# Optimization experiments

Hardware: AMD Instinct MI355X
Metric: run time of the kernel (lower is better)

The kernel has to match this reference:

```python
import jax, jax.numpy as jnp
import numpy as np

B, T, C = 4, 2048, 1024
H = 16
D = C // H  # head_dim = 64


def setup_inputs() -> dict:
    key = jax.random.key(0)
    k1, k2, k3, k4, k5 = jax.random.split(key, 5)
    s = 1.0 / np.sqrt(C)
    return {
        "hidden_state": jax.random.normal(k1, (B, T, C), dtype=jnp.float32),
        "qkv_w": jax.random.uniform(k2, (C, 3 * C), jnp.float32, -s, s),
        "qkv_b": jax.random.uniform(k3, (3 * C,), jnp.float32, -s, s),
        "o_w": jax.random.uniform(k4, (C, C), jnp.float32, -s, s),
        "o_b": jax.random.uniform(k5, (C,), jnp.float32, -s, s),
    }


def reference(hidden_state, qkv_w, qkv_b, o_w, o_b):
    Bq, Tq, Cq = hidden_state.shape
    qkv = hidden_state @ qkv_w + qkv_b  # [B,T,3C]
    q, k, v = jnp.split(qkv, 3, axis=-1)
    # [B,T,C] -> [B,H,T,D]
    q = q.reshape(Bq, Tq, H, D).transpose(0, 2, 1, 3)
    k = k.reshape(Bq, Tq, H, D).transpose(0, 2, 1, 3)
    v = v.reshape(Bq, Tq, H, D).transpose(0, 2, 1, 3)
    scaling = D ** (-0.5)
    scores = jnp.einsum("bhqd,bhkd->bhqk", q, k) * scaling  # [B,H,T,T]
    causal = jnp.tril(jnp.ones((Tq, Tq), dtype=bool))
    scores = jnp.where(causal[None, None], scores, -jnp.inf)
    attn = jax.nn.softmax(scores, axis=-1)
    out = jnp.einsum("bhqk,bhkd->bhqd", attn, v)  # [B,H,T,D]
    out = out.transpose(0, 2, 1, 3).reshape(Bq, Tq, Cq)
    return out @ o_w + o_b
```

## Files before the change

kernel.cpp:

```cpp
#include <hip/hip_runtime.h>
#include <hip/hip_bf16.h>

#define Bn 4
#define Tn 2048
#define Cn 1024
#define Hn 16
#define Dn 64
#define Kdim 1024

typedef __bf16 bf16x8 __attribute__((ext_vector_type(8)));
typedef float f32x4 __attribute__((ext_vector_type(4)));
union B8 { uint4 u; bf16x8 f; ushort s[8]; };

static __device__ __forceinline__ ushort f2bf(float x) {
    __hip_bfloat16 h = __float2bfloat16(x);
    return *(ushort*)&h;
}

#define AS1 __attribute__((address_space(1)))
#define AS3 __attribute__((address_space(3)))

static __device__ __forceinline__ void gload_lds16(const ushort* g, ushort* l) {
    __builtin_amdgcn_global_load_lds((AS1 const uint4*)(const void*)g,
                                     (AS3 uint4*)(void*)l, 16, 0, 0);
}

__global__ __launch_bounds__(256) void cvt_bf16(
    const float* __restrict__ src, ushort* __restrict__ dst, int n)
{
    int i = (blockIdx.x * 256 + threadIdx.x) * 8;
    if (i >= n) return;
    float4 a = *(const float4*)&src[i];
    float4 b = *(const float4*)&src[i + 4];
    ushort4 o0, o1;
    o0.x = f2bf(a.x); o0.y = f2bf(a.y); o0.z = f2bf(a.z); o0.w = f2bf(a.w);
    o1.x = f2bf(b.x); o1.y = f2bf(b.y); o1.z = f2bf(b.z); o1.w = f2bf(b.w);
    *(ushort4*)&dst[i] = o0;
    *(ushort4*)&dst[i + 4] = o1;
}

__global__ __launch_bounds__(256) void transpose_bf16(
    const float* __restrict__ W, ushort* __restrict__ Wt, int N)
{
    __shared__ float Ls[32][33];
    const int k0 = blockIdx.y * 32, n0 = blockIdx.x * 32;
    const int tx = threadIdx.x & 31, ty = threadIdx.x >> 5;
    #pragma unroll
    for (int i = 0; i < 4; i++) {
        int r = ty + i * 8;
        Ls[r][tx] = W[(size_t)(k0 + r) * N + n0 + tx];
    }
    __syncthreads();
    #pragma unroll
    for (int i = 0; i < 4; i++) {
        int r = ty + i * 8;
        Wt[(size_t)(n0 + r) * Kdim + k0 + tx] = f2bf(Ls[tx][r]);
    }
}

template <int EPI>
__global__ __launch_bounds__(256) void gemm_bt(
    const ushort* __restrict__ A, const ushort* __restrict__ Bt,
    const float* __restrict__ bias,
    float* __restrict__ Out, ushort* __restrict__ Qb,
    ushort* __restrict__ Kb, ushort* __restrict__ Vtb)
{
    const int m0 = blockIdx.y * 128;
    const int n0 = blockIdx.x * 128;
    const int t  = threadIdx.x;
    const int wave = t >> 6, lane = t & 63;
    const int ln = lane & 15, quad = lane >> 4;
    const int wm = wave >> 1, wn = wave & 1;

    __shared__ ushort As[128 * 64];
    __shared__ ushort Bs[128 * 64];

    f32x4 acc[4][4] = {};

    for (int k0 = 0; k0 < Kdim; k0 += 64) {
        __syncthreads();
        #pragma unroll
        for (int it = 0; it < 4; it++) {
            int c = it * 256 + wave * 64 + lane;
            int row = c >> 3, seg = c & 7;
            int gseg = seg ^ (row & 7);
            gload_lds16(&A [(size_t)(m0 + row) * Kdim + k0 + gseg * 8], &As[c * 8]);
            gload_lds16(&Bt[(size_t)(n0 + row) * Kdim + k0 + gseg * 8], &Bs[c * 8]);
        }
        __syncthreads();

        #pragma unroll
        for (int ks = 0; ks < 2; ks++) {
            bf16x8 af[4], bf[4];
            #pragma unroll
            for (int mm = 0; mm < 4; mm++) {
                int row = wm * 64 + mm * 16 + ln;
                int seg = (ks * 4 + quad) ^ (ln & 7);
                B8 tmp; tmp.u = *(const uint4*)&As[row * 64 + seg * 8];
                af[mm] = tmp.f;
            }
            #pragma unroll
            for (int nn = 0; nn < 4; nn++) {
                int row = wn * 64 + nn * 16 + ln;
                int seg = (ks * 4 + quad) ^ (ln & 7);
                B8 tmp; tmp.u = *(const uint4*)&Bs[row * 64 + seg * 8];
                bf[nn] = tmp.f;
            }
            #pragma unroll
            for (int mm = 0; mm < 4; mm++)
                #pragma unroll
                for (int nn = 0; nn < 4; nn++)
                    acc[mm][nn] = __builtin_amdgcn_mfma_f32_16x16x32_bf16(
                        af[mm], bf[nn], acc[mm][nn], 0, 0, 0);
        }
    }

    if (EPI == 0) {
        #pragma unroll
        for (int nn = 0; nn < 4; nn++) {
            int n = n0 + wn * 64 + nn * 16 + ln;
            float bv = bias[n];
            #pragma unroll
            for (int mm = 0; mm < 4; mm++) {
                int mbase = m0 + wm * 64 + mm * 16 + quad * 4;
                #pragma unroll
                for (int reg = 0; reg < 4; reg++)
                    Out[(size_t)(mbase + reg) * 1024 + n] = acc[mm][nn][reg] + bv;
            }
        }
    } else {
        const int nb = n0 + wn * 64;
        const int which = nb >> 10;
        const int h = (nb & 1023) >> 6;
        const float scale = (which == 0) ? 0.125f * 1.44269504088896f : 1.0f;
        const int b_ = m0 >> 11;
        const int t0 = (m0 & 2047) + wm * 64;

        __syncthreads();
        ushort* tile = ((wave & 2) ? Bs : As) + (wave & 1) * 4096;

        if (which == 2) {
            #pragma unroll
            for (int nn = 0; nn < 4; nn++) {
                float bv = bias[nb + nn * 16 + ln];
                #pragma unroll
                for (int mm = 0; mm < 4; mm++)
                    #pragma unroll
                    for (int reg = 0; reg < 4; reg++) {
                        int m = mm * 16 + quad * 4 + reg;
                        int n = nn * 16 + ln;
                        tile[n * 64 + (m ^ (((n >> 1) & 7) * 8))] =
                            f2bf(acc[mm][nn][reg] + bv);
                    }
            }
            #pragma unroll
            for (int it = 0; it < 8; it++) {
                int idx = it * 64 + lane;
                int row = idx >> 3, seg = idx & 7;
                uint4 v = *(const uint4*)&tile[row * 64 +
                              ((seg * 8) ^ (((row >> 1) & 7) * 8))];
                *(uint4*)&Vtb[((size_t)((b_ * Hn + h) * Dn) + row) * Tn + t0 + seg * 8] = v;
            }
        } else {
            ushort* dst = (which == 0) ? Qb : Kb;
            #pragma unroll
            for (int nn = 0; nn < 4; nn++) {
                float bv = bias[nb + nn * 16 + ln];
                #pragma unroll
                for (int mm = 0; mm < 4; mm++)
                    #pragma unroll
                    for (int reg = 0; reg < 4; reg++) {
                        int m = mm * 16 + quad * 4 + reg;
                        int n = nn * 16 + ln;
                        tile[m * 64 + (n ^ (((m >> 1) & 7) * 8))] =
                            f2bf((acc[mm][nn][reg] + bv) * scale);
                    }
            }
            #pragma unroll
            for (int it = 0; it < 8; it++) {
                int idx = it * 64 + lane;
                int row = idx >> 3, seg = idx & 7;
                uint4 v = *(const uint4*)&tile[row * 64 +
                              ((seg * 8) ^ (((row >> 1) & 7) * 8))];
                *(uint4*)&dst[((size_t)((b_ * Hn + h) * Tn) + t0 + row) * Dn + seg * 8] = v;
            }
        }
    }
}

__global__ __launch_bounds__(256, 2) void attn_mfma(
    const ushort* __restrict__ Qb, const ushort* __restrict__ Kb,
    const ushort* __restrict__ Vtb, ushort* __restrict__ Ob)
{
    const int bh   = blockIdx.x;
    const int qt   = 15 - blockIdx.y;
    const int t    = threadIdx.x;
    const int wave = t >> 6, lane = t & 63;
    const int ln   = lane & 15, quad = lane >> 4;

    __shared__ ushort Ks[2][128 * 64];
    __shared__ ushort Ps[4][32 * 34];

    const ushort* KgB = Kb  + (size_t)bh * Tn * Dn;
    const ushort* VgB = Vtb + (size_t)bh * Dn * Tn;
    const int b_ = bh >> 4, h = bh & 15;

    #define STAGE_K(kc, buf)                                                   \
        do {                                                                   \
            _Pragma("unroll")                                                  \
            for (int it = 0; it < 4; it++) {                                   \
                int c = it * 256 + wave * 64 + lane;                           \
                int row = c >> 3, seg = c & 7;                                 \
                int gs = seg ^ (row & 7);                                      \
                gload_lds16(&KgB[(size_t)((kc) * 128 + row) * Dn + gs * 8],    \
                            &Ks[buf][c * 8]);                                  \
            }                                                                  \
        } while (0)

    int cur = 0;
    STAGE_K(0, 0);

    const int q0 = qt * 128;

    const ushort* Qg = Qb + ((size_t)bh * Tn + q0 + wave * 32) * Dn;
    bf16x8 qf[2][2];
    #pragma unroll
    for (int ns = 0; ns < 2; ns++)
        #pragma unroll
        for (int ks = 0; ks < 2; ks++) {
            B8 tmp; tmp.u = *(const uint4*)&Qg[(ns * 16 + ln) * 64 + ks * 32 + quad * 8];
            qf[ns][ks] = tmp.f;
        }

    f32x4 Oacc[4][2] = {};
    float m_r[2] = {-1e30f, -1e30f}, l_r[2] = {0.f, 0.f};

    for (int kc = 0; kc <= qt; kc++) {
        __syncthreads();

        B8 vfr[4][4];
        #pragma unroll
        for (int gks = 0; gks < 4; gks++)
            #pragma unroll
            for (int ctd = 0; ctd < 4; ctd++)
                vfr[ctd][gks].u = *(const uint4*)&VgB[
                    (size_t)(ctd * 16 + ln) * Tn + kc * 128 + gks * 32 + quad * 8];

        if (kc < qt) STAGE_K(kc + 1, cur ^ 1);

        const ushort* Kc = Ks[cur];
        f32x4 S[8][2] = {};
        #pragma unroll
        for (int ks = 0; ks < 2; ks++)
            #pragma unroll
            for (int ct = 0; ct < 8; ct++) {
                B8 a; a.u = *(const uint4*)&Kc[(ct * 16 + ln) * 64 +
                                               (((ks * 4 + quad) ^ (ln & 7)) * 8)];
                #pragma unroll
                for (int ns = 0; ns < 2; ns++)
                    S[ct][ns] = __builtin_amdgcn_mfma_f32_16x16x32_bf16(
                        a.f, qf[ns][ks], S[ct][ns], 0, 0, 0);
            }

        if (kc == qt) {
            #pragma unroll
            for (int ct = 0; ct < 8; ct++) {
                int keyl = ct * 16 + quad * 4;
                #pragma unroll
                for (int ns = 0; ns < 2; ns++) {
                    int ql = wave * 32 + ns * 16 + ln;
                    #pragma unroll
                    for (int reg = 0; reg < 4; reg++)
                        if (keyl + reg > ql) S[ct][ns][reg] = -1e30f;
                }
            }
        }

        float alpha[2], ssum[2] = {0.f, 0.f};
        #pragma unroll
        for (int ns = 0; ns < 2; ns++) {
            float pm = -1e30f;
            #pragma unroll
            for (int ct = 0; ct < 8; ct++)
                #pragma unroll
                for (int reg = 0; reg < 4; reg++)
                    pm = fmaxf(pm, S[ct][ns][reg]);
            pm = fmaxf(pm, __shfl_xor(pm, 16));
            pm = fmaxf(pm, __shfl_xor(pm, 32));
            float mn = fmaxf(m_r[ns], pm);
            alpha[ns] = exp2f(m_r[ns] - mn);
            m_r[ns] = mn;
            #pragma unroll
            for (int ctd = 0; ctd < 4; ctd++)
                Oacc[ctd][ns] *= alpha[ns];
        }

        ushort* Pw = Ps[wave];
        #pragma unroll
        for (int p = 0; p < 4; p++) {
            #pragma unroll
            for (int ct_h = 0; ct_h < 2; ct_h++) {
                int ct = p * 2 + ct_h;
                #pragma unroll
                for (int ns = 0; ns < 2; ns++) {
                    ushort4 o;
                    #pragma unroll
                    for (int reg = 0; reg < 4; reg++) {
                        float pv = exp2f(S[ct][ns][reg] - m_r[ns]);
                        ssum[ns] += pv;
                        ((ushort*)&o)[reg] = f2bf(pv);
                    }
                    *(ushort4*)&Pw[(ns * 16 + ln) * 34 + ct_h * 16 + quad * 4] = o;
                }
            }
            #pragma unroll
            for (int ns = 0; ns < 2; ns++) {
                B8 pfr; pfr.u = *(const uint4*)&Pw[(ns * 16 + ln) * 34 + quad * 8];
                #pragma unroll
                for (int ctd = 0; ctd < 4; ctd++)
                    Oacc[ctd][ns] = __builtin_amdgcn_mfma_f32_16x16x32_bf16(
                        vfr[ctd][p].f, pfr.f, Oacc[ctd][ns], 0, 0, 0);
            }
        }
        #pragma unroll
        for (int ns = 0; ns < 2; ns++) {
            float s = ssum[ns];
            s += __shfl_xor(s, 16);
            s += __shfl_xor(s, 32);
            l_r[ns] = l_r[ns] * alpha[ns] + s;
        }
        cur ^= 1;
    }

    #pragma unroll
    for (int ns = 0; ns < 2; ns++) {
        float inv = 1.0f / l_r[ns];
        int token = q0 + wave * 32 + ns * 16 + ln;
        ushort* dst = Ob + ((size_t)(b_ * Tn + token)) * Cn + h * 64;
        #pragma unroll
        for (int ctd = 0; ctd < 4; ctd++) {
            ushort4 o;
            #pragma unroll
            for (int reg = 0; reg < 4; reg++)
                ((ushort*)&o)[reg] = f2bf(Oacc[ctd][ns][reg] * inv);
            *(ushort4*)&dst[ctd * 16 + quad * 4] = o;
        }
    }
    #undef STAGE_K
}

extern "C" void kernel_launch(void* const* d_in, const int* in_sizes, int n_in,
                              void* d_out, int out_size, void* d_ws, size_t ws_size,
                              hipStream_t stream) {
    const float* X     = (const float*)d_in[0];
    const float* qkv_w = (const float*)d_in[1];
    const float* qkv_b = (const float*)d_in[2];
    const float* o_w   = (const float*)d_in[3];
    const float* o_b   = (const float*)d_in[4];
    float* out = (float*)d_out;

    const size_t BTC = (size_t)Bn * Tn * Cn;
    ushort* Xb  = (ushort*)d_ws;
    ushort* Wqt = Xb  + BTC;
    ushort* Wot = Wqt + 3 * Cn * Cn;
    ushort* Qb  = Wot + Cn * Cn;
    ushort* Kb  = Qb  + BTC;
    ushort* Vtb = Kb  + BTC;
    ushort* Ao  = Vtb + BTC;

    cvt_bf16<<<dim3((int)(BTC / 8 / 256)), 256, 0, stream>>>(X, Xb, (int)BTC);
    transpose_bf16<<<dim3(3 * Cn / 32, Kdim / 32), 256, 0, stream>>>(qkv_w, Wqt, 3 * Cn);
    transpose_bf16<<<dim3(Cn / 32, Kdim / 32), 256, 0, stream>>>(o_w, Wot, Cn);

    gemm_bt<1><<<dim3(3 * Cn / 128, 8192 / 128), 256, 0, stream>>>(
        Xb, Wqt, qkv_b, nullptr, Qb, Kb, Vtb);
    attn_mfma<<<dim3(Bn * Hn, 16), 256, 0, stream>>>(Qb, Kb, Vtb, Ao);
    gemm_bt<0><<<dim3(Cn / 128, 8192 / 128), 256, 0, stream>>>(
        Ao, Wot, o_b, out, nullptr, nullptr, nullptr);
}
```

Before: 310.9 us.

## Feed P to PV MFMA from registers via 16x16x16 bf16, dropping LDS round-trip

Replaces the per-wave LDS staging of the softmax probabilities with direct register reuse. The S accumulator layout of the 16x16 MFMA output matches the B-operand layout of the 16x16x16 bf16 MFMA, so P values are packed to bf16 in registers and fed straight into the PV product. V fragments are reloaded as 4-element chunks to match. This removes LDS writes, reads and the P shared buffer, at the cost of twice as many smaller MFMA instructions and more, narrower V global loads.

```diff
diff --git a/kernel.cpp b/kernel.cpp
--- a/kernel.cpp
+++ b/kernel.cpp
@@ -9,12 +9,29 @@
 #define Kdim 1024
 
 typedef __bf16 bf16x8 __attribute__((ext_vector_type(8)));
+typedef __bf16 bf16x4 __attribute__((ext_vector_type(4)));
+typedef short s16x4 __attribute__((ext_vector_type(4)));
 typedef float f32x4 __attribute__((ext_vector_type(4)));
 union B8 { uint4 u; bf16x8 f; ushort s[8]; };
+union B4 { uint2 u; s16x4 s; bf16x4 f; ushort h[4]; };
 
 static __device__ __forceinline__ ushort f2bf(float x) {
     __hip_bfloat16 h = __float2bfloat16(x);
     return *(ushort*)&h;
+}
+static __device__ __forceinline__ uint pk2bf(float lo, float hi) {
+    return (uint)f2bf(lo) | ((uint)f2bf(hi) << 16);
+}
+
+static __device__ __forceinline__ f32x4 pv_mfma(B4 a, B4 b, f32x4 c) {
+#if __has_builtin(__builtin_amdgcn_mfma_f32_16x16x16bf16_1k)
+    return __builtin_amdgcn_mfma_f32_16x16x16bf16_1k(a.s, b.s, c, 0, 0, 0);
+#elif __has_builtin(__builtin_amdgcn_mfma_f32_16x16x16_bf16)
+    return __builtin_amdgcn_mfma_f32_16x16x16_bf16(a.f, b.f, c, 0, 0, 0);
+#else
+    asm("v_mfma_f32_16x16x16_bf16 %0, %1, %2, %0" : "+v"(c) : "v"(a.u), "v"(b.u));
+    return c;
+#endif
 }
 
 #define AS1 __attribute__((address_space(1)))
@@ -199,7 +216,6 @@
     const int ln   = lane & 15, quad = lane >> 4;
 
     __shared__ ushort Ks[2][128 * 64];
-    __shared__ ushort Ps[4][32 * 34];
 
     const ushort* KgB = Kb  + (size_t)bh * Tn * Dn;
     const ushort* VgB = Vtb + (size_t)bh * Dn * Tn;
@@ -238,13 +254,13 @@
     for (int kc = 0; kc <= qt; kc++) {
         __syncthreads();
 
-        B8 vfr[4][4];
-        #pragma unroll
-        for (int gks = 0; gks < 4; gks++)
+        B4 vfr[8][4];
+        #pragma unroll
+        for (int ct = 0; ct < 8; ct++)
             #pragma unroll
             for (int ctd = 0; ctd < 4; ctd++)
-                vfr[ctd][gks].u = *(const uint4*)&VgB[
-                    (size_t)(ctd * 16 + ln) * Tn + kc * 128 + gks * 32 + quad * 8];
+                vfr[ct][ctd].u = *(const uint2*)&VgB[
+                    (size_t)(ctd * 16 + ln) * Tn + kc * 128 + ct * 16 + quad * 4];
 
         if (kc < qt) STAGE_K(kc + 1, cur ^ 1);
 
@@ -295,31 +311,21 @@
                 Oacc[ctd][ns] *= alpha[ns];
         }
 
-        ushort* Pw = Ps[wave];
-        #pragma unroll
-        for (int p = 0; p < 4; p++) {
-            #pragma unroll
-            for (int ct_h = 0; ct_h < 2; ct_h++) {
-                int ct = p * 2 + ct_h;
-                #pragma unroll
-                for (int ns = 0; ns < 2; ns++) {
-                    ushort4 o;
-                    #pragma unroll
-                    for (int reg = 0; reg < 4; reg++) {
-                        float pv = exp2f(S[ct][ns][reg] - m_r[ns]);
-                        ssum[ns] += pv;
-                        ((ushort*)&o)[reg] = f2bf(pv);
-                    }
-                    *(ushort4*)&Pw[(ns * 16 + ln) * 34 + ct_h * 16 + quad * 4] = o;
-                }
-            }
+        #pragma unroll
+        for (int ct = 0; ct < 8; ct++) {
             #pragma unroll
             for (int ns = 0; ns < 2; ns++) {
-                B8 pfr; pfr.u = *(const uint4*)&Pw[(ns * 16 + ln) * 34 + quad * 8];
+                float p0 = exp2f(S[ct][ns][0] - m_r[ns]);
+                float p1 = exp2f(S[ct][ns][1] - m_r[ns]);
+                float p2 = exp2f(S[ct][ns][2] - m_r[ns]);
+                float p3 = exp2f(S[ct][ns][3] - m_r[ns]);
+                ssum[ns] += (p0 + p1) + (p2 + p3);
+                B4 pb;
+                pb.u.x = pk2bf(p0, p1);
+                pb.u.y = pk2bf(p2, p3);
                 #pragma unroll
                 for (int ctd = 0; ctd < 4; ctd++)
-                    Oacc[ctd][ns] = __builtin_amdgcn_mfma_f32_16x16x32_bf16(
-                        vfr[ctd][p].f, pfr.f, Oacc[ctd][ns], 0, 0, 0);
+                    Oacc[ctd][ns] = pv_mfma(vfr[ct][ctd], pb, Oacc[ctd][ns]);
             }
         }
         #pragma unroll
```

Result: slower. 342.0 us (+10.0%).
